# Kernel tuning notes

Hardware: AMD Instinct MI355X
Metric: run time of the kernel (lower is better)

The kernel has to match this reference:

```python
import jax, jax.numpy as jnp
import numpy as np

N_NODES = 50000
N_EDGES = 800000
D = 64  # in_dim == hidden_dim == out_dim
BN_EPS = 1e-5


def setup_inputs() -> dict:
    key = jax.random.key(0)
    ks = jax.random.split(key, 12)
    x = jax.random.normal(ks[0], (N_NODES, D), dtype=jnp.float32)
    edge_index = jax.random.randint(ks[1], (2, N_EDGES), 0, N_NODES, dtype=jnp.int64)
    scale = 1.0 / np.sqrt(D)
    W1 = jax.random.normal(ks[2], (D, D), dtype=jnp.float32) * scale
    b1 = jnp.zeros((D,), jnp.float32)
    W2 = jax.random.normal(ks[3], (D, D), dtype=jnp.float32) * scale
    b2 = jnp.zeros((D,), jnp.float32)
    W3 = jax.random.normal(ks[4], (D, D), dtype=jnp.float32) * scale
    b3 = jnp.zeros((D,), jnp.float32)
    # BatchNorm (eval mode: running stats) params for the two hidden layers
    g1 = jnp.ones((D,), jnp.float32); be1 = jnp.zeros((D,), jnp.float32)
    m1 = jax.random.normal(ks[5], (D,), dtype=jnp.float32) * 0.1
    v1 = jax.random.uniform(ks[6], (D,), dtype=jnp.float32, minval=0.5, maxval=1.5)
    g2 = jnp.ones((D,), jnp.float32); be2 = jnp.zeros((D,), jnp.float32)
    m2 = jax.random.normal(ks[7], (D,), dtype=jnp.float32) * 0.1
    v2 = jax.random.uniform(ks[8], (D,), dtype=jnp.float32, minval=0.5, maxval=1.5)
    return {"x": x, "edge_index": edge_index,
            "W1": W1, "b1": b1, "g1": g1, "be1": be1, "m1": m1, "v1": v1,
            "W2": W2, "b2": b2, "g2": g2, "be2": be2, "m2": m2, "v2": v2,
            "W3": W3, "b3": b3}


def reference(x, edge_index, W1, b1, g1, be1, m1, v1,
              W2, b2, g2, be2, m2, v2, W3, b3):
    N = x.shape[0]
    loop = jnp.arange(N, dtype=edge_index.dtype)
    src = jnp.concatenate([edge_index[0], loop])  # [E+N]
    dst = jnp.concatenate([edge_index[1], loop])
    # GCN symmetric normalization: deg over dst (with self loops)
    deg = jax.ops.segment_sum(jnp.ones(dst.shape, x.dtype), dst, num_segments=N)
    dinv = jnp.where(deg > 0, jax.lax.rsqrt(deg), 0.0)
    norm = (dinv[src] * dinv[dst])[:, None]  # [E+N, 1]

    def gcn_conv(h, W, b):
        h = h @ W  # linear transform first (PyG GCNConv order)
        return jax.ops.segment_sum(h[src] * norm, dst, num_segments=N) + b

    def bn(h, g, be, m, v):  # eval-mode BatchNorm1d
        return (h - m) * jax.lax.rsqrt(v + BN_EPS) * g + be

    h = jax.nn.relu(bn(gcn_conv(x, W1, b1), g1, be1, m1, v1))
    h = jax.nn.relu(bn(gcn_conv(h, W2, b2), g2, be2, m2, v2))
    return gcn_conv(h, W3, b3)
```

## Files before the change

### kernel.cpp

```cpp
#include <hip/hip_runtime.h>
#include <hip/hip_fp16.h>

#define D 64
#define BN_EPS 1e-5f
typedef unsigned short u16;
typedef unsigned int u32;

#define NB_MAX 256
#define A3_EDGES 4096

__global__ __launch_bounds__(256) void k_setup(
    const void* __restrict__ ei, int N, int* __restrict__ flag,
    int* __restrict__ bucketCnt,
    const float* __restrict__ g1, const float* __restrict__ be1,
    const float* __restrict__ m1, const float* __restrict__ v1,
    const float* __restrict__ g2, const float* __restrict__ be2,
    const float* __restrict__ m2, const float* __restrict__ v2,
    float* __restrict__ bn) {
    int d = threadIdx.x;
    bucketCnt[d] = 0;
    if (d < 64) {
        float s = g1[d] * rsqrtf(v1[d] + BN_EPS);
        bn[d] = s; bn[64 + d] = be1[d] - m1[d] * s;
        float q = g2[d] * rsqrtf(v2[d] + BN_EPS);
        bn[128 + d] = q; bn[192 + d] = be2[d] - m2[d] * q;
    } else if (d == 64) {
        const long long* p = (const long long*)ei;
        int ok = 1;
        for (int j = 0; j < 16; ++j) {
            long long v = p[j];
            if (v < 0 || v >= (long long)N) { ok = 0; break; }
        }
        *flag = ok;
    }
}

__device__ __forceinline__ int get_idx(const void* ei, int is64, int pos) {
    if (is64) return (int)((const long long*)ei)[pos];
    return ((const int*)ei)[pos];
}

__global__ __launch_bounds__(256) void k_bucket_count(
    const void* __restrict__ ei, const int* __restrict__ flag, int E, int nb,
    int* __restrict__ bucketCnt) {
    __shared__ int hist[NB_MAX];
    for (int i = threadIdx.x; i < nb; i += 256) hist[i] = 0;
    __syncthreads();
    const int is64 = *flag;
    for (int e = blockIdx.x * 256 + threadIdx.x; e < E; e += gridDim.x * 256)
        atomicAdd(&hist[get_idx(ei, is64, E + e) >> 8], 1);
    __syncthreads();
    for (int i = threadIdx.x; i < nb; i += 256)
        if (hist[i]) atomicAdd(&bucketCnt[i], hist[i]);
}

__global__ __launch_bounds__(256) void k_bucket_scan(
    const int* __restrict__ bucketCnt, int nb, int* __restrict__ bucketOff,
    int* __restrict__ bucketCur, int* __restrict__ rowptr, int N, int E) {
    __shared__ int s[256];
    int tid = threadIdx.x;
    int v = (tid < nb) ? bucketCnt[tid] : 0;
    s[tid] = v; __syncthreads();
    for (int off = 1; off < 256; off <<= 1) {
        int t = (tid >= off) ? s[tid - off] : 0;
        __syncthreads(); s[tid] += t; __syncthreads();
    }
    if (tid < nb) { bucketOff[tid] = s[tid] - v; bucketCur[tid] = 0; }
    if (tid == nb) bucketOff[nb] = E;
    if (tid == 0) rowptr[N] = E;
}

__global__ __launch_bounds__(256) void k_bucket_scatter(
    const void* __restrict__ ei, const int* __restrict__ flag, int E, int nb,
    const int* __restrict__ bucketOff, int* __restrict__ bucketCur,
    u32* __restrict__ staged) {
    __shared__ u32 recs[A3_EDGES];
    __shared__ int hist[NB_MAX];
    __shared__ int lpos[NB_MAX];
    __shared__ int gbase[NB_MAX];
    const int tid = threadIdx.x;
    const int base = blockIdx.x * A3_EDGES;
    const int cnt = min(A3_EDGES, E - base);
    const int is64 = *flag;
    for (int i = tid; i < nb; i += 256) hist[i] = 0;
    __syncthreads();
    u32 myrec[16];
    const int per = (cnt + 255) >> 8;
    for (int j = 0; j < per; ++j) {
        int o = j * 256 + tid;
        if (o < cnt) {
            int e = base + o;
            u32 src = (u32)get_idx(ei, is64, e);
            u32 dst = (u32)get_idx(ei, is64, E + e);
            u32 bkt = dst >> 8;
            myrec[j] = (bkt << 24) | (src << 8) | (dst & 255u);
            atomicAdd(&hist[bkt], 1);
        } else myrec[j] = 0xffffffffu;
    }
    __syncthreads();
    int v = (tid < nb) ? hist[tid] : 0;
    lpos[tid] = v; __syncthreads();
    for (int off = 1; off < 256; off <<= 1) {
        int t = (tid >= off) ? lpos[tid - off] : 0;
        __syncthreads(); lpos[tid] += t; __syncthreads();
    }
    int excl = lpos[tid] - v;
    if (tid < nb && v > 0) gbase[tid] = atomicAdd(&bucketCur[tid], v);
    __syncthreads();
    if (tid < nb) { lpos[tid] = excl; hist[tid] = 0; }
    __syncthreads();
    for (int j = 0; j < per; ++j) {
        u32 r = myrec[j];
        if (r != 0xffffffffu) {
            int b = (int)(r >> 24);
            int p = lpos[b] + atomicAdd(&hist[b], 1);
            recs[p] = r;
        }
    }
    __syncthreads();
    const int wave = tid >> 6, lane = tid & 63;
    for (int b = wave; b < nb; b += 4) {
        int c = hist[b]; if (!c) continue;
        int gdst = bucketOff[b] + gbase[b];
        int lsrc = lpos[b];
        for (int k = lane; k < c; k += 64) staged[gdst + k] = recs[lsrc + k];
    }
}

__global__ __launch_bounds__(256) void k_bucket_build(
    const u32* __restrict__ staged, const int* __restrict__ bucketOff,
    int* __restrict__ rowptr, float* __restrict__ dinv, u16* __restrict__ csr,
    int N) {
    __shared__ int hist[256], off[256], cur[256];
    const int b = blockIdx.x, tid = threadIdx.x;
    const int beg = bucketOff[b], end = bucketOff[b + 1];
    hist[tid] = 0;
    __syncthreads();
    for (int i = beg + tid; i < end; i += 256)
        atomicAdd(&hist[staged[i] & 255u], 1);
    __syncthreads();
    int v = hist[tid];
    off[tid] = v; __syncthreads();
    for (int o = 1; o < 256; o <<= 1) {
        int t = (tid >= o) ? off[tid - o] : 0;
        __syncthreads(); off[tid] += t; __syncthreads();
    }
    int excl = off[tid] - v;
    const int dst = b * 256 + tid;
    if (dst < N) { rowptr[dst] = beg + excl; dinv[dst] = rsqrtf(1.0f + (float)v); }
    __syncthreads();
    off[tid] = excl; cur[tid] = 0;
    __syncthreads();
    for (int i = beg + tid; i < end; i += 256) {
        u32 r = staged[i];
        int dl = (int)(r & 255u);
        int p = beg + off[dl] + atomicAdd(&cur[dl], 1);
        csr[p] = (u16)((r >> 8) & 0xffffu);
    }
}

#define GROWS 64
__global__ __launch_bounds__(256) void k_gemm(
    const float* __restrict__ h, const float* __restrict__ W,
    const float* __restrict__ dinv, __half* __restrict__ h2s, int N) {
    __shared__ float hs[GROWS * 65];
    __shared__ float Ws[64 * 64];
    const int tid = threadIdx.x;
    const int row0 = blockIdx.x * GROWS;
    const int nrow = min(GROWS, N - row0);
    const float4* Wp = (const float4*)W;
    float4* Wsp = (float4*)Ws;
    for (int i = tid; i < 1024; i += 256) Wsp[i] = Wp[i];
    const float4* hp = (const float4*)h + (size_t)row0 * 16;
    for (int i = tid; i < nrow * 16; i += 256) {
        float4 t = hp[i];
        int r = i >> 4, c4 = (i & 15) << 2;
        float* dp = &hs[r * 65 + c4];
        dp[0] = t.x; dp[1] = t.y; dp[2] = t.z; dp[3] = t.w;
    }
    __syncthreads();
    const int r = tid >> 2, q = tid & 3;
    const int row = row0 + r;
    if (r >= nrow) return;
    float out[16];
#pragma unroll
    for (int c = 0; c < 16; ++c) out[c] = 0.f;
    for (int k = 0; k < 64; ++k) {
        float a = hs[r * 65 + k];
        const float* Wk = &Ws[k * 64 + q * 16];
#pragma unroll
        for (int c = 0; c < 16; ++c) out[c] = fmaf(a, Wk[c], out[c]);
    }
    const float di = dinv[row];
    u32 pk[8];
#pragma unroll
    for (int c = 0; c < 8; ++c) {
        u32 lo = __half_as_ushort(__float2half(di * out[2 * c]));
        u32 hi = __half_as_ushort(__float2half(di * out[2 * c + 1]));
        pk[c] = (hi << 16) | lo;
    }
    uint4* op = (uint4*)(h2s + (size_t)row * 64 + q * 16);
    op[0] = make_uint4(pk[0], pk[1], pk[2], pk[3]);
    op[1] = make_uint4(pk[4], pk[5], pk[6], pk[7]);
}

__device__ __forceinline__ void acc8(float* acc, const float4& v) {
    const __half2* hv = (const __half2*)&v;
#pragma unroll
    for (int q2 = 0; q2 < 4; ++q2) {
        float2 t = __half22float2(hv[q2]);
        acc[2 * q2] += t.x; acc[2 * q2 + 1] += t.y;
    }
}

template <int MODE>
__global__ __launch_bounds__(256) void k_gather(
    const int* __restrict__ rowptr, const u16* __restrict__ csr,
    const __half* __restrict__ h2s, const float* __restrict__ dinv,
    const float* __restrict__ b, const float* __restrict__ bn, int bn_off,
    const float* __restrict__ Wn, __half* __restrict__ h2o,
    float* __restrict__ outp, int N, int E) {
    __shared__ float ytile[4][64];
    const int nd = threadIdx.x >> 6;
    const int node = blockIdx.x * 4 + nd;
    const int lane = threadIdx.x & 63;
    const int g = lane >> 3;
    const int f = lane & 7;
    float acc[8];
#pragma unroll
    for (int k = 0; k < 8; ++k) acc[k] = 0.f;

    if (node < N) {
        const int beg = rowptr[node], end = rowptr[node + 1];
        float4 sv = ((const float4*)(h2s + (size_t)node * 64))[f];
        if (g == 0) acc8(acc, sv);

        for (int c = beg; c < end; c += 64) {
            int p = c + lane;
            int idx = csr[p < E ? p : (E - 1)];
            const int navail = min(64, end - c);
            const int nj = (navail + 7) >> 3;
            int j = 0;
            for (; j + 2 <= nj; j += 2) {
                int s0 = __shfl(idx, j * 8 + g);
                int s1 = __shfl(idx, j * 8 + 8 + g);
                float4 v0 = ((const float4*)(h2s + (size_t)s0 * 64))[f];
                float4 v1 = ((const float4*)(h2s + (size_t)s1 * 64))[f];
                if (j * 8 + g < navail) acc8(acc, v0);
                if (j * 8 + 8 + g < navail) acc8(acc, v1);
            }
            if (j < nj) {
                int s0 = __shfl(idx, j * 8 + g);
                float4 v0 = ((const float4*)(h2s + (size_t)s0 * 64))[f];
                if (j * 8 + g < navail) acc8(acc, v0);
            }
        }
#pragma unroll
        for (int m = 8; m <= 32; m <<= 1) {
#pragma unroll
            for (int k = 0; k < 8; ++k) acc[k] += __shfl_xor(acc[k], m);
        }
        const float dn = dinv[node];
        float bb[8], y[8];
        ((float4*)bb)[0] = ((const float4*)b)[2 * f];
        ((float4*)bb)[1] = ((const float4*)b)[2 * f + 1];
#pragma unroll
        for (int k = 0; k < 8; ++k) y[k] = dn * acc[k] + bb[k];
        if (MODE == 0) {
            float ss[8], tt[8];
            ((float4*)ss)[0] = ((const float4*)(bn + bn_off))[2 * f];
            ((float4*)ss)[1] = ((const float4*)(bn + bn_off))[2 * f + 1];
            ((float4*)tt)[0] = ((const float4*)(bn + bn_off + 64))[2 * f];
            ((float4*)tt)[1] = ((const float4*)(bn + bn_off + 64))[2 * f + 1];
#pragma unroll
            for (int k = 0; k < 8; ++k) y[k] = fmaxf(y[k] * ss[k] + tt[k], 0.f);
            if (g == 0) {
                float4* yt = (float4*)&ytile[nd][f * 8];
                yt[0] = make_float4(y[0], y[1], y[2], y[3]);
                yt[1] = make_float4(y[4], y[5], y[6], y[7]);
            }
        } else {
            if (g == 0) {
                float4* op = (float4*)(outp + (size_t)node * 64 + f * 8);
                op[0] = make_float4(y[0], y[1], y[2], y[3]);
                op[1] = make_float4(y[4], y[5], y[6], y[7]);
            }
        }
    }
    if (MODE == 0) {
        __syncthreads();
        if (node < N) {
            const int col = lane;
            float z = 0.f;
#pragma unroll 8
            for (int k = 0; k < 64; ++k) z = fmaf(ytile[nd][k], Wn[k * 64 + col], z);
            h2o[(size_t)node * 64 + col] = __float2half(dinv[node] * z);
        }
    }
}

extern "C" void kernel_launch(void* const* d_in, const int* in_sizes, int n_in,
                              void* d_out, int out_size, void* d_ws, size_t ws_size,
                              hipStream_t stream) {
    const float* x  = (const float*)d_in[0];
    const void*  ei = d_in[1];
    const float* W1 = (const float*)d_in[2];
    const float* b1 = (const float*)d_in[3];
    const float* g1 = (const float*)d_in[4];
    const float* be1= (const float*)d_in[5];
    const float* m1 = (const float*)d_in[6];
    const float* v1 = (const float*)d_in[7];
    const float* W2 = (const float*)d_in[8];
    const float* b2 = (const float*)d_in[9];
    const float* g2 = (const float*)d_in[10];
    const float* be2= (const float*)d_in[11];
    const float* m2 = (const float*)d_in[12];
    const float* v2 = (const float*)d_in[13];
    const float* W3 = (const float*)d_in[14];
    const float* b3 = (const float*)d_in[15];

    const int N = in_sizes[0] / D;
    const int E = in_sizes[1] / 2;
    const int nb = (N + 255) >> 8;
    float* out = (float*)d_out;

    char* ws = (char*)d_ws;
    int*   flag      = (int*)ws;
    float* bn        = (float*)(ws + 256);
    int*   bucketCnt = (int*)(ws + 2048);
    int*   bucketOff = (int*)(ws + 4096);
    int*   bucketCur = (int*)(ws + 8192);
    int*   rowptr    = (int*)(ws + 12288);
    float* dinv      = (float*)(ws + 12288 + 200192);
    u32*   staged    = (u32*)(ws + 12288 + 2 * 200192);
    u16*   csr       = (u16*)((char*)staged + (size_t)E * 4 + 256);
    __half* bufA     = (__half*)((char*)csr + (size_t)E * 2 + 256);
    __half* bufC     = bufA + (size_t)N * D;

    const int gGemm = (N + GROWS - 1) / GROWS;
    const int gGath = (N + 3) / 4;
    const int gA3   = (E + A3_EDGES - 1) / A3_EDGES;

    k_setup<<<1, 256, 0, stream>>>(ei, N, flag, bucketCnt,
                                   g1, be1, m1, v1, g2, be2, m2, v2, bn);
    k_bucket_count<<<256, 256, 0, stream>>>(ei, flag, E, nb, bucketCnt);
    k_bucket_scan<<<1, 256, 0, stream>>>(bucketCnt, nb, bucketOff, bucketCur,
                                         rowptr, N, E);
    k_bucket_scatter<<<gA3, 256, 0, stream>>>(ei, flag, E, nb, bucketOff,
                                              bucketCur, staged);
    k_bucket_build<<<nb, 256, 0, stream>>>(staged, bucketOff, rowptr, dinv, csr, N);

    k_gemm<<<gGemm, 256, 0, stream>>>(x, W1, dinv, bufA, N);
    k_gather<0><<<gGath, 256, 0, stream>>>(rowptr, csr, bufA, dinv, b1, bn, 0,
                                           W2, bufC, nullptr, N, E);
    k_gather<0><<<gGath, 256, 0, stream>>>(rowptr, csr, bufC, dinv, b2, bn, 128,
                                           W3, bufA, nullptr, N, E);
    k_gather<1><<<gGath, 256, 0, stream>>>(rowptr, csr, bufA, dinv, b3, bn, 0,
                                           nullptr, nullptr, out, N, E);
}
```

Baseline: 186.9 us.

## Assign 16 lanes per node in gather and vectorize the fused next-layer GEMV

The gather kernel moves from one 64-lane wavefront per node to 16 lanes per node, so a 256-thread block covers 16 nodes. Each 16-lane group loads 16 neighbour indices at a time and issues 8 independent float4 loads per lane, and the cross-lane reduction shrinks to a single xor-shuffle. This is meant to fit the average degree of about 17 better, so fewer lanes idle on partial 64-wide chunks. The fused transform by the next weight matrix now gives each thread 4 output columns, read from W with float4 loads and written back as packed half stores. In exchange, per-thread register use rises from the 8-entry load buffer, and high-degree nodes take more serial iterations.

```diff
diff --git a/kernel.cpp b/kernel.cpp
--- a/kernel.cpp
+++ b/kernel.cpp
@@ -220,12 +220,15 @@
     const float* __restrict__ b, const float* __restrict__ bn, int bn_off,
     const float* __restrict__ Wn, __half* __restrict__ h2o,
     float* __restrict__ outp, int N, int E) {
-    __shared__ float ytile[4][64];
-    const int nd = threadIdx.x >> 6;
-    const int node = blockIdx.x * 4 + nd;
-    const int lane = threadIdx.x & 63;
-    const int g = lane >> 3;
+    __shared__ float ytile[16][68];
+    const int tid = threadIdx.x;
+    const int lane = tid & 63;
+    const int n16 = tid >> 4;
+    const int node = blockIdx.x * 16 + n16;
+    const int g2 = (lane >> 3) & 1;
     const int f = lane & 7;
+    const int lbase = lane & ~15;
+
     float acc[8];
 #pragma unroll
     for (int k = 0; k < 8; ++k) acc[k] = 0.f;
@@ -233,54 +236,46 @@
     if (node < N) {
         const int beg = rowptr[node], end = rowptr[node + 1];
         float4 sv = ((const float4*)(h2s + (size_t)node * 64))[f];
-        if (g == 0) acc8(acc, sv);
-
-        for (int c = beg; c < end; c += 64) {
-            int p = c + lane;
-            int idx = csr[p < E ? p : (E - 1)];
-            const int navail = min(64, end - c);
-            const int nj = (navail + 7) >> 3;
-            int j = 0;
-            for (; j + 2 <= nj; j += 2) {
-                int s0 = __shfl(idx, j * 8 + g);
-                int s1 = __shfl(idx, j * 8 + 8 + g);
-                float4 v0 = ((const float4*)(h2s + (size_t)s0 * 64))[f];
-                float4 v1 = ((const float4*)(h2s + (size_t)s1 * 64))[f];
-                if (j * 8 + g < navail) acc8(acc, v0);
-                if (j * 8 + 8 + g < navail) acc8(acc, v1);
+        if (g2 == 0) acc8(acc, sv);
+
+        for (int c = beg; c < end; c += 16) {
+            int p = c + (lane & 15);
+            int idx = csr[p < E ? p : E - 1];
+            const int navail = min(16, end - c);
+            float4 v[8];
+            int e[8];
+#pragma unroll
+            for (int j = 0; j < 8; ++j) {
+                e[j] = 2 * j + g2;
+                int s = __shfl(idx, lbase + e[j]);
+                v[j] = ((const float4*)(h2s + (size_t)s * 64))[f];
             }
-            if (j < nj) {
-                int s0 = __shfl(idx, j * 8 + g);
-                float4 v0 = ((const float4*)(h2s + (size_t)s0 * 64))[f];
-                if (j * 8 + g < navail) acc8(acc, v0);
-            }
-        }
-#pragma unroll
-        for (int m = 8; m <= 32; m <<= 1) {
-#pragma unroll
-            for (int k = 0; k < 8; ++k) acc[k] += __shfl_xor(acc[k], m);
-        }
-        const float dn = dinv[node];
-        float bb[8], y[8];
-        ((float4*)bb)[0] = ((const float4*)b)[2 * f];
-        ((float4*)bb)[1] = ((const float4*)b)[2 * f + 1];
-#pragma unroll
-        for (int k = 0; k < 8; ++k) y[k] = dn * acc[k] + bb[k];
-        if (MODE == 0) {
-            float ss[8], tt[8];
-            ((float4*)ss)[0] = ((const float4*)(bn + bn_off))[2 * f];
-            ((float4*)ss)[1] = ((const float4*)(bn + bn_off))[2 * f + 1];
-            ((float4*)tt)[0] = ((const float4*)(bn + bn_off + 64))[2 * f];
-            ((float4*)tt)[1] = ((const float4*)(bn + bn_off + 64))[2 * f + 1];
-#pragma unroll
-            for (int k = 0; k < 8; ++k) y[k] = fmaxf(y[k] * ss[k] + tt[k], 0.f);
-            if (g == 0) {
-                float4* yt = (float4*)&ytile[nd][f * 8];
+#pragma unroll
+            for (int j = 0; j < 8; ++j)
+                if (e[j] < navail) acc8(acc, v[j]);
+        }
+#pragma unroll
+        for (int k = 0; k < 8; ++k) acc[k] += __shfl_xor(acc[k], 8);
+
+        if (g2 == 0) {
+            const float dn = dinv[node];
+            float bb[8], y[8];
+            ((float4*)bb)[0] = ((const float4*)b)[2 * f];
+            ((float4*)bb)[1] = ((const float4*)b)[2 * f + 1];
+#pragma unroll
+            for (int k = 0; k < 8; ++k) y[k] = dn * acc[k] + bb[k];
+            if (MODE == 0) {
+                float ss[8], tt[8];
+                ((float4*)ss)[0] = ((const float4*)(bn + bn_off))[2 * f];
+                ((float4*)ss)[1] = ((const float4*)(bn + bn_off))[2 * f + 1];
+                ((float4*)tt)[0] = ((const float4*)(bn + bn_off + 64))[2 * f];
+                ((float4*)tt)[1] = ((const float4*)(bn + bn_off + 64))[2 * f + 1];
+#pragma unroll
+                for (int k = 0; k < 8; ++k) y[k] = fmaxf(y[k] * ss[k] + tt[k], 0.f);
+                float4* yt = (float4*)&ytile[n16][f * 8];
                 yt[0] = make_float4(y[0], y[1], y[2], y[3]);
                 yt[1] = make_float4(y[4], y[5], y[6], y[7]);
-            }
-        } else {
-            if (g == 0) {
+            } else {
                 float4* op = (float4*)(outp + (size_t)node * 64 + f * 8);
                 op[0] = make_float4(y[0], y[1], y[2], y[3]);
                 op[1] = make_float4(y[4], y[5], y[6], y[7]);
@@ -290,11 +285,21 @@
     if (MODE == 0) {
         __syncthreads();
         if (node < N) {
-            const int col = lane;
-            float z = 0.f;
-#pragma unroll 8
-            for (int k = 0; k < 64; ++k) z = fmaf(ytile[nd][k], Wn[k * 64 + col], z);
-            h2o[(size_t)node * 64 + col] = __float2half(dinv[node] * z);
+            const int cq = (tid & 15) << 2;
+            float z0 = 0.f, z1 = 0.f, z2 = 0.f, z3 = 0.f;
+#pragma unroll 4
+            for (int k = 0; k < 64; ++k) {
+                float a = ytile[n16][k];
+                float4 w = *(const float4*)(Wn + k * 64 + cq);
+                z0 = fmaf(a, w.x, z0); z1 = fmaf(a, w.y, z1);
+                z2 = fmaf(a, w.z, z2); z3 = fmaf(a, w.w, z3);
+            }
+            const float dn = dinv[node];
+            u32 p0 = ((u32)__half_as_ushort(__float2half(dn * z1)) << 16)
+                   | __half_as_ushort(__float2half(dn * z0));
+            u32 p1 = ((u32)__half_as_ushort(__float2half(dn * z3)) << 16)
+                   | __half_as_ushort(__float2half(dn * z2));
+            *(uint2*)(h2o + (size_t)node * 64 + cq) = make_uint2(p0, p1);
         }
     }
 }
@@ -338,7 +343,7 @@
     __half* bufC     = bufA + (size_t)N * D;
 
     const int gGemm = (N + GROWS - 1) / GROWS;
-    const int gGath = (N + 3) / 4;
+    const int gGath = (N + 15) / 16;
     const int gA3   = (E + A3_EDGES - 1) / A3_EDGES;
 
     k_setup<<<1, 256, 0, stream>>>(ei, N, flag, bucketCnt,
```

After: 165.9 us. 11.2% less time.
